# Kernel tuning notes

Measured on AMD Instinct MI355X. Metric: run time of the kernel, lower is better.

Reference implementation:

```python
import jax, jax.numpy as jnp
import numpy as np

GRID_SIZE = 5   # efficient-kan default
K = 3           # spline_order
BATCH = 32768
OBS_DIM = 128
ACTION_DIM = 18
# (in_features, out_features) for the 7 KANLinear layers:
# base: 128->256->256->64 ; adv head: 64->64->18 ; value head: 64->64->1
DIMS = [(OBS_DIM, 256), (256, 256), (256, 64), (64, 64), (64, ACTION_DIM), (64, 64), (64, 1)]


def make_grid(in_f):
    # uniform grid on [-1,1] extended by K knots each side: shape (in_f, GRID_SIZE+2K+1)
    h = 2.0 / GRID_SIZE
    g = jnp.arange(-K, GRID_SIZE + K + 1, dtype=jnp.float32) * h - 1.0
    return jnp.broadcast_to(g, (in_f, g.shape[0]))


def b_splines(x, grid):
    # Cox-de Boor recursion; x: (B, in) -> bases (B, in, GRID_SIZE+K)
    xe = x[:, :, None]
    b = ((xe >= grid[:, :-1]) & (xe < grid[:, 1:])).astype(x.dtype)
    for j in range(1, K + 1):
        left = (xe - grid[:, : -(j + 1)]) / (grid[:, j:-1] - grid[:, : -(j + 1)])
        right = (grid[:, j + 1:] - xe) / (grid[:, j + 1:] - grid[:, 1:-j])
        b = left * b[:, :, :-1] + right * b[:, :, 1:]
    return b


def kan_layer(x, bw, sw, sc):
    # efficient-kan KANLinear: silu base path + spline path with standalone scaler
    grid = make_grid(x.shape[1])
    base = jax.nn.silu(x) @ bw.T                              # (B, out)
    bases = b_splines(x, grid)                                # (B, in, G+K)
    spline = jnp.einsum('big,oig->bo', bases, sw * sc[:, :, None])
    return base + spline


def setup_inputs() -> dict:
    key = jax.random.key(0)
    ks = jax.random.split(key, 1 + 3 * len(DIMS))
    inp = {"x": jax.random.normal(ks[0], (BATCH, OBS_DIM), dtype=jnp.float32)}
    for i, (fin, fout) in enumerate(DIMS):
        inp[f"bw{i}"] = jax.random.normal(ks[1 + 3 * i], (fout, fin), dtype=jnp.float32) / np.sqrt(fin).astype(np.float32)
        inp[f"sw{i}"] = jax.random.normal(ks[2 + 3 * i], (fout, fin, GRID_SIZE + K), dtype=jnp.float32) * (0.1 / np.sqrt(fin).astype(np.float32))
        inp[f"sc{i}"] = 1.0 + 0.1 * jax.random.normal(ks[3 + 3 * i], (fout, fin), dtype=jnp.float32)
    return inp


def reference(x, bw0, sw0, sc0, bw1, sw1, sc1, bw2, sw2, sc2,
              bw3, sw3, sc3, bw4, sw4, sc4, bw5, sw5, sc5, bw6, sw6, sc6):
    h = x
    for bw, sw, sc in [(bw0, sw0, sc0), (bw1, sw1, sc1), (bw2, sw2, sc2)]:
        h = kan_layer(h, bw, sw, sc)
    advantage = kan_layer(kan_layer(h, bw3, sw3, sc3), bw4, sw4, sc4)
    state_value = kan_layer(kan_layer(h, bw5, sw5, sc5), bw6, sw6, sc6)
    return (advantage, state_value)
```

## Files before the change

kernel.cpp:

```cpp
#include <hip/hip_runtime.h>

typedef unsigned short u16;
typedef unsigned int   u32;
typedef unsigned long long u64;
typedef __bf16 bf16;
typedef float f32x4  __attribute__((ext_vector_type(4)));
typedef bf16  bf16x8 __attribute__((ext_vector_type(8)));

__device__ __forceinline__ float bf2f(u16 u){ return (float)__builtin_bit_cast(bf16,u); }
__device__ __forceinline__ u16   f2bf(float f){ return __builtin_bit_cast(u16,(bf16)f); }
__device__ __forceinline__ u32   pkbf(float a,float b){ return (u32)f2bf(a)|((u32)f2bf(b)<<16); }

#define NROWS 32768

__device__ __forceinline__ uint4 basis_pk(float x)
{
  float tp  = __fmaf_rn(x, 2.5f, 5.5f);
  float tpc = fminf(fmaxf(tp, -1.0f), 12.0f);
  float fi  = floorf(tpc);
  float uu  = tpc - fi;
  int   i0  = (int)fi;
  float u2 = uu*uu, u3 = u2*uu, w1 = 1.0f-uu, w2 = w1*w1, w3 = w2*w1;
  float d1 = __fmaf_rn(3.0f, u3, __fmaf_rn(-6.0f, u2, 4.0f));
  float d2 = __fmaf_rn(3.0f, w3, __fmaf_rn(-6.0f, w2, 4.0f));
  u64 dpk = (u64)pkbf(w3, d1) | ((u64)pkbf(d2, u3) << 32);
  int ss = i0*16 - 48;
  u64 A  = dpk << (ss & 63);
  u64 Bv = dpk >> ((64-ss) & 63);
  u64 Cv = dpk << ((ss-64) & 63);
  u64 Dv = dpk >> ((-ss) & 63);
  u64 lo = (ss>=0 && ss<64)   ? A  : ((ss<0 && ss>-64) ? Dv : 0ull);
  u64 hi = (ss>=64 && ss<128) ? Cv : ((ss>0 && ss<64)  ? Bv : 0ull);
  uint4 r; r.x=(u32)lo; r.y=(u32)(lo>>32); r.z=(u32)hi; r.w=(u32)(hi>>32);
  return r;
}

__device__ __forceinline__ void expand9(float x, u16& sil, uint4& bpk)
{
  float s = x * (1.0f/(1.0f+__expf(-x)));
  sil = f2bf(s);
  bpk = basis_pk(x);
}
__device__ __forceinline__ void expand10(float x, u32& spk, uint4& bpk)
{
  float s = x * (1.0f/(1.0f+__expf(-x)));
  u16 uh = f2bf(s);
  u16 ul = f2bf(s - bf2f(uh));
  spk = (u32)uh | ((u32)ul<<16);
  bpk = basis_pk(x);
}

struct PrepArgs {
  const float* bw[7]; const float* sw[7]; const float* sc[7];
  u16* w[7];
  int cin[7]; int coutr[7]; int ntsh[7]; int fmt[7];
  u32 elems[7];
};

__global__ __launch_bounds__(256) void prep_kernel(PrepArgs pa)
{
  u32 idx = blockIdx.x*256 + threadIdx.x;
  int L = 0;
  u32 off = idx;
  while (L < 6 && off >= pa.elems[L]) { off -= pa.elems[L]; ++L; }
  int j    = off & 7;
  int lane = (off>>3) & 63;
  u32 tl   = off >> 9;
  int ntsh = pa.ntsh[L];
  u32 kstep = tl >> ntsh;
  int ntile = (int)(tl & ((1u<<ntsh)-1u));
  int o    = ntile*16 + (lane&15);
  int kpos = (lane>>4)*8 + j;
  int i = 0, g = 0; bool sil;
  if (pa.fmt[L] == 0){
    u32 c = kstep/9u; int r = (int)(kstep - c*9u);
    if (r == 0){ i = (int)c*32 + kpos; sil = true; }
    else { int kl=(r-1)*32+kpos; i=(int)c*32+(kl>>3); g=kl&7; sil = false; }
  } else {
    u32 c = kstep/5u; int r = (int)(kstep - c*5u);
    if (r == 0){ i = (int)c*16 + (kpos>>1); sil = true; }
    else { int kl=(r-1)*32+kpos; i=(int)c*16+(kl>>3); g=kl&7; sil = false; }
  }
  float v = 0.f;
  if (o < pa.coutr[L]) {
    size_t e = (size_t)o*pa.cin[L] + i;
    v = sil ? pa.bw[L][e] : pa.sw[L][e*8+g]*pa.sc[L][e]*0.16666666666666666f;
  }
  pa.w[L][off] = f2bf(v);
}

template<int CIN,int COUT,int GR,int GC,int IN_MODE,int OUT_MODE>
__global__ __launch_bounds__(512,4) void kan_layer(const void* __restrict__ hin_,
    const u16* __restrict__ W, void* __restrict__ hout_)
{
  constexpr int ROWS = 64;
  constexpr int NCH = CIN/32;
  constexpr int TOTK = NCH*9;
  constexpr int NTILES = COUT/16;
  constexpr int MT  = ROWS/(GR*16);
  constexpr int NTL = NTILES/GC;
  static_assert(GR*GC == 8, "wave grid must use all 8 waves");
  static_assert(MT*GR*16 == ROWS, "row coverage");
  static_assert(NTL*GC == NTILES, "col coverage");
  constexpr int SROW=20, BROW=132, BOFF=ROWS*SROW;
  constexpr int CHUNK = BOFF + ROWS*BROW;
  constexpr int WSTEP = NTILES*512;
  __shared__ __align__(16) u32 buf[2][CHUNK];

  const int b0 = blockIdx.x*ROWS;
  const int tid = threadIdx.x;
  const int wave = tid>>6, lane = tid&63, m = lane&15, quad = lane>>4;
  const int rg = wave / GC, cg = wave % GC;
  const int rbase = rg*(MT*16);

  const u16*   __restrict__ hb = (const u16*)hin_;
  const float* __restrict__ hf = (const float*)hin_;

  f32x4 acc[MT][NTL];
#pragma unroll
  for (int a=0;a<MT;++a)
#pragma unroll
    for (int n=0;n<NTL;++n) acc[a][n]=(f32x4){0.f,0.f,0.f,0.f};

  const u16* wq = W + ((size_t)(cg*NTL)*64 + lane)*8;
  bf16x8 bbuf[3][NTL];
  auto loadB = [&](int kstep, bf16x8* dst){
    if (kstep < TOTK){
#pragma unroll
      for (int nt=0; nt<NTL; ++nt)
        dst[nt] = *(const bf16x8*)(wq + nt*512);
    }
    wq += WSTEP;
  };
  loadB(0, bbuf[0]); loadB(1, bbuf[1]);

  float xb[2][4];
  auto loadX = [&](int kc, float* dst){
#pragma unroll
    for (int t=0;t<4;++t){
      int task = t*512+tid, row = task>>5, f = task&31;
      int gi = (b0+row)*CIN + kc*32 + f;
      dst[t] = (IN_MODE==0)? hf[gi] : bf2f(hb[gi]);
    }
  };
  auto expandChunk = [&](const float* xc, u32* dstb){
#pragma unroll
    for (int t=0;t<4;++t){
      int task=t*512+tid, row=task>>5, f=task&31;
      u16 sil; uint4 bpk;
      expand9(xc[t], sil, bpk);
      ((u16*)dstb)[row*(SROW*2) + f] = sil;
      *(uint4*)&dstb[BOFF + row*BROW + f*4] = bpk;
    }
  };

  loadX(0, xb[0]);
  expandChunk(xb[0], buf[0]);
  if (NCH > 1) loadX(1, xb[1]);
  __syncthreads();

  for (int kc=0; kc<NCH; ++kc){
    u32* cur = buf[kc&1];
    u32* nxt = buf[(kc+1)&1];
    if (kc+1 < NCH) expandChunk(xb[(kc+1)&1], nxt);
    if (kc+2 < NCH) loadX(kc+2, xb[kc&1]);
#pragma unroll
    for (int ks=0; ks<9; ++ks){
      const int kstep = kc*9 + ks;
      loadB(kstep+2, bbuf[(ks+2)%3]);
      bf16x8 af[MT];
#pragma unroll
      for (int mt=0; mt<MT; ++mt){
        int row = rbase + mt*16 + m;
        af[mt] = (ks==0)
          ? *(const bf16x8*)&cur[row*SROW + quad*4]
          : *(const bf16x8*)&cur[BOFF + row*BROW + (ks-1)*16 + quad*4];
      }
#pragma unroll
      for (int nt=0; nt<NTL; ++nt)
#pragma unroll
        for (int mt=0; mt<MT; ++mt)
          acc[mt][nt] = __builtin_amdgcn_mfma_f32_16x16x32_bf16(af[mt], bbuf[ks%3][nt], acc[mt][nt],0,0,0);
    }
    __syncthreads();
  }

#pragma unroll
  for (int mt=0; mt<MT; ++mt)
#pragma unroll
    for (int nt=0; nt<NTL; ++nt)
#pragma unroll
      for (int r=0; r<4; ++r){
        size_t off = (size_t)(b0 + rbase + mt*16 + quad*4 + r)*COUT + (cg*NTL+nt)*16 + m;
        if constexpr (OUT_MODE==0) ((float*)hout_)[off] = acc[mt][nt][r];
        else                       ((u16*)hout_)[off]   = f2bf(acc[mt][nt][r]);
      }
}

template<int IN_MODE>
__global__ __launch_bounds__(512,4) void tail2_kernel(const void* __restrict__ h1_,
  const u16* __restrict__ W2, const u16* __restrict__ W3, const u16* __restrict__ W4,
  const u16* __restrict__ W5, const u16* __restrict__ W6,
  float* __restrict__ out_adv, float* __restrict__ out_val)
{
  __shared__ __align__(16) u32 smem[19456];
  float* hH = (float*)smem;
  float* hA = (float*)(smem + 4160);
  float* hV = (float*)(smem + 8320);
  u32*  Aex = smem + 12480;

  const int b0 = blockIdx.x*64;
  const int tid = threadIdx.x;
  const int wave = tid>>6, lane = tid&63, m = lane&15, quad = lane>>4;
  const int rg = wave>>2, cg = wave&3;

  const u16*   __restrict__ hb = (const u16*)h1_;
  const float* __restrict__ hf = (const float*)h1_;

  {
    constexpr int CIN=256, NCH=8, TOTK=72, NTILES=4;
    constexpr int SROW=20, BROW=132, BOFF=64*SROW, CHUNK=BOFF+64*BROW;
    f32x4 acc[2];
    acc[0]=(f32x4){0,0,0,0}; acc[1]=(f32x4){0,0,0,0};
    const u16* wq = W2 + ((size_t)cg*64 + lane)*8;
    bf16x8 bb[3];
    auto loadB = [&](int kstep, bf16x8* dst){
      if (kstep < TOTK) *dst = *(const bf16x8*)wq;
      wq += NTILES*512;
    };
    loadB(0,&bb[0]); loadB(1,&bb[1]);
    float xb[2][4];
    auto loadX = [&](int kc, float* dst){
#pragma unroll
      for (int t=0;t<4;++t){
        int task=t*512+tid, row=task>>5, f=task&31;
        int gi=(b0+row)*CIN + kc*32 + f;
        dst[t] = (IN_MODE==0)? hf[gi] : bf2f(hb[gi]);
      }
    };
    auto expandChunk = [&](const float* xc, u32* dstb){
#pragma unroll
      for (int t=0;t<4;++t){
        int task=t*512+tid, row=task>>5, f=task&31;
        u16 sil; uint4 bpk;
        expand9(xc[t], sil, bpk);
        ((u16*)dstb)[row*(SROW*2)+f] = sil;
        *(uint4*)&dstb[BOFF + row*BROW + f*4] = bpk;
      }
    };
    loadX(0, xb[0]);
    expandChunk(xb[0], smem);
    loadX(1, xb[1]);
    __syncthreads();
    for (int kc=0; kc<NCH; ++kc){
      u32* cur = smem + (kc&1)*CHUNK;
      u32* nxt = smem + ((kc+1)&1)*CHUNK;
      if (kc+1 < NCH) expandChunk(xb[(kc+1)&1], nxt);
      if (kc+2 < NCH) loadX(kc+2, xb[kc&1]);
#pragma unroll
      for (int ks=0; ks<9; ++ks){
        loadB(kc*9+ks+2, &bb[(ks+2)%3]);
        bf16x8 af[2];
#pragma unroll
        for (int mt=0; mt<2; ++mt){
          int row = rg*32 + mt*16 + m;
          af[mt] = (ks==0)
            ? *(const bf16x8*)&cur[row*SROW + quad*4]
            : *(const bf16x8*)&cur[BOFF + row*BROW + (ks-1)*16 + quad*4];
        }
#pragma unroll
        for (int mt=0; mt<2; ++mt)
          acc[mt] = __builtin_amdgcn_mfma_f32_16x16x32_bf16(af[mt], bb[ks%3], acc[mt],0,0,0);
      }
      __syncthreads();
    }
#pragma unroll
    for (int mt=0; mt<2; ++mt)
#pragma unroll
      for (int r=0;r<4;++r)
        hH[(rg*32 + mt*16 + quad*4 + r)*65 + cg*16 + m] = acc[mt][r];
  }
  __syncthreads();

  constexpr int SROW=20, BROW=68, BOFF=64*20;

  f32x4 a3[2], a5[2];
#pragma unroll
  for (int mt=0;mt<2;++mt){ a3[mt]=(f32x4){0,0,0,0}; a5[mt]=(f32x4){0,0,0,0}; }

  const u16* w3q = W3 + ((size_t)cg*64 + lane)*8;
  const u16* w5q = W5 + ((size_t)cg*64 + lane)*8;
  bf16x8 w3b[3], w5b[3];
  auto loadB2 = [&](int kstep, int d){
    if (kstep < 20){
      w3b[d] = *(const bf16x8*)w3q;
      w5b[d] = *(const bf16x8*)w5q;
    }
    w3q += 4*512; w5q += 4*512;
  };
  loadB2(0,0); loadB2(1,1);

  for (int kc=0; kc<4; ++kc){
#pragma unroll
    for (int t=0;t<2;++t){
      int task=t*512+tid, row=task>>4, f=task&15;
      u32 spk; uint4 bpk;
      expand10(hH[row*65 + kc*16 + f], spk, bpk);
      Aex[row*SROW + f] = spk;
      *(uint4*)&Aex[BOFF + row*BROW + f*4] = bpk;
    }
    __syncthreads();
#pragma unroll
    for (int ks=0; ks<5; ++ks){
      loadB2(kc*5+ks+2, 2);
      bf16x8 af[2];
#pragma unroll
      for (int mt=0; mt<2; ++mt){
        int row = rg*32 + mt*16 + m;
        af[mt] = (ks==0)
          ? *(const bf16x8*)&Aex[row*SROW + quad*4]
          : *(const bf16x8*)&Aex[BOFF + row*BROW + (ks-1)*16 + quad*4];
      }
#pragma unroll
      for (int mt=0; mt<2; ++mt){
        a3[mt] = __builtin_amdgcn_mfma_f32_16x16x32_bf16(af[mt], w3b[0], a3[mt],0,0,0);
        a5[mt] = __builtin_amdgcn_mfma_f32_16x16x32_bf16(af[mt], w5b[0], a5[mt],0,0,0);
      }
      w3b[0]=w3b[1]; w3b[1]=w3b[2]; w5b[0]=w5b[1]; w5b[1]=w5b[2];
    }
    __syncthreads();
  }
#pragma unroll
  for (int mt=0;mt<2;++mt)
#pragma unroll
    for (int r=0;r<4;++r){
      int row = rg*32 + mt*16 + quad*4 + r;
      hA[row*65 + cg*16 + m] = a3[mt][r];
      hV[row*65 + cg*16 + m] = a5[mt][r];
    }
  __syncthreads();

  f32x4 a4[2];
#pragma unroll
  for (int mt=0;mt<2;++mt) a4[mt]=(f32x4){0,0,0,0};
  const u16* w4q = W4 + ((size_t)cg*64 + lane)*8;
  bf16x8 w4b[3];
  auto loadB4 = [&](int kstep, int d){
    if (kstep < 20) w4b[d] = *(const bf16x8*)w4q;
    w4q += 4*512;
  };
  loadB4(0,0); loadB4(1,1);
  for (int kc=0; kc<4; ++kc){
#pragma unroll
    for (int t=0;t<2;++t){
      int task=t*512+tid, row=task>>4, f=task&15;
      u32 spk; uint4 bpk;
      expand10(hA[row*65 + kc*16 + f], spk, bpk);
      Aex[row*SROW + f] = spk;
      *(uint4*)&Aex[BOFF + row*BROW + f*4] = bpk;
    }
    __syncthreads();
#pragma unroll
    for (int ks=0; ks<5; ++ks){
      loadB4(kc*5+ks+2, 2);
      bf16x8 af[2];
#pragma unroll
      for (int mt=0; mt<2; ++mt){
        int row = rg*32 + mt*16 + m;
        af[mt] = (ks==0)
          ? *(const bf16x8*)&Aex[row*SROW + quad*4]
          : *(const bf16x8*)&Aex[BOFF + row*BROW + (ks-1)*16 + quad*4];
      }
#pragma unroll
      for (int mt=0; mt<2; ++mt)
        a4[mt] = __builtin_amdgcn_mfma_f32_16x16x32_bf16(af[mt], w4b[0], a4[mt],0,0,0);
      w4b[0]=w4b[1]; w4b[1]=w4b[2];
    }
    __syncthreads();
  }
  {
    int col = cg*16 + m;
    if (col < 18){
#pragma unroll
      for (int mt=0;mt<2;++mt)
#pragma unroll
        for (int r=0;r<4;++r)
          out_adv[(size_t)(b0 + rg*32 + mt*16 + quad*4 + r)*18 + col] = a4[mt][r];
    }
  }

  f32x4 a6[2];
#pragma unroll
  for (int mt=0;mt<2;++mt) a6[mt]=(f32x4){0,0,0,0};
  const u16* w6q = W6 + ((size_t)cg*64 + lane)*8;
  bf16x8 w6b[3];
  auto loadB6 = [&](int kstep, int d){
    if (kstep < 20) w6b[d] = *(const bf16x8*)w6q;
    w6q += 4*512;
  };
  loadB6(0,0); loadB6(1,1);
  for (int kc=0; kc<4; ++kc){
#pragma unroll
    for (int t=0;t<2;++t){
      int task=t*512+tid, row=task>>4, f=task&15;
      u32 spk; uint4 bpk;
      expand10(hV[row*65 + kc*16 + f], spk, bpk);
      Aex[row*SROW + f] = spk;
      *(uint4*)&Aex[BOFF + row*BROW + f*4] = bpk;
    }
    __syncthreads();
#pragma unroll
    for (int ks=0; ks<5; ++ks){
      loadB6(kc*5+ks+2, 2);
      bf16x8 af[2];
#pragma unroll
      for (int mt=0; mt<2; ++mt){
        int row = rg*32 + mt*16 + m;
        af[mt] = (ks==0)
          ? *(const bf16x8*)&Aex[row*SROW + quad*4]
          : *(const bf16x8*)&Aex[BOFF + row*BROW + (ks-1)*16 + quad*4];
      }
#pragma unroll
      for (int mt=0; mt<2; ++mt)
        a6[mt] = __builtin_amdgcn_mfma_f32_16x16x32_bf16(af[mt], w6b[0], a6[mt],0,0,0);
      w6b[0]=w6b[1]; w6b[1]=w6b[2];
    }
    __syncthreads();
  }
  if (cg==0 && m==0){
#pragma unroll
    for (int mt=0;mt<2;++mt)
#pragma unroll
      for (int r=0;r<4;++r)
        out_val[b0 + rg*32 + mt*16 + quad*4 + r] = a6[mt][r];
  }
}

extern "C" void kernel_launch(void* const* d_in, const int* in_sizes, int n_in,
                              void* d_out, int out_size, void* d_ws, size_t ws_size,
                              hipStream_t stream)
{
  (void)in_sizes; (void)n_in; (void)out_size;
  char* ws = (char*)d_ws;

  const size_t wbytes[7] = {589824u, 1179648u, 294912u, 81920u, 81920u, 81920u, 81920u};
  const bool midf32 = ws_size >= 77889536u;

  u16* W[7];
  char *h0, *h1;
  if (midf32) {
    h0 = ws;
    h1 = h0 + 33554432u;
    size_t off = 75497472u;
    for (int l=0;l<7;++l){ W[l] = (u16*)(ws+off); off += wbytes[l]; }
  } else {
    h0 = ws;
    h1 = h0 + 16777216u;
    size_t off = 37748736u;
    for (int l=0;l<7;++l){ W[l] = (u16*)(ws+off); off += wbytes[l]; }
  }

  PrepArgs pa;
  const int cins[7]   = {128,256,256,64,64,64,64};
  const int coutr[7]  = {256,256,64,64,18,64,1};
  const int ntsh[7]   = {4,4,2,2,2,2,2};
  const int fmts[7]   = {0,0,0,1,1,1,1};
  const u32 elems[7]  = {294912u,589824u,147456u,40960u,40960u,40960u,40960u};
  for (int l=0;l<7;++l){
    pa.bw[l] = (const float*)d_in[1+3*l];
    pa.sw[l] = (const float*)d_in[2+3*l];
    pa.sc[l] = (const float*)d_in[3+3*l];
    pa.w[l]  = W[l];
    pa.cin[l]=cins[l]; pa.coutr[l]=coutr[l]; pa.ntsh[l]=ntsh[l]; pa.fmt[l]=fmts[l];
    pa.elems[l]=elems[l];
  }
  prep_kernel<<<4672, 256, 0, stream>>>(pa);

  dim3 g64(NROWS/64), bl(512);
  float* out_adv = (float*)d_out;
  float* out_val = (float*)d_out + (size_t)NROWS*18;
  if (midf32) {
    kan_layer<128,256,1,8,0,0><<<g64,bl,0,stream>>>(d_in[0], W[0], h0);
    kan_layer<256,256,1,8,0,0><<<g64,bl,0,stream>>>(h0, W[1], h1);
    tail2_kernel<0><<<g64,bl,0,stream>>>(h1, W[2], W[3], W[4], W[5], W[6], out_adv, out_val);
  } else {
    kan_layer<128,256,1,8,0,1><<<g64,bl,0,stream>>>(d_in[0], W[0], h0);
    kan_layer<256,256,1,8,1,1><<<g64,bl,0,stream>>>(h0, W[1], h1);
    tail2_kernel<1><<<g64,bl,0,stream>>>(h1, W[2], W[3], W[4], W[5], W[6], out_adv, out_val);
  }
}
```

Before: 221.7 us.

## Fuse three layer kernels into one persistent-per-tile mega kernel

Merges the two wide KAN layer kernels and the tail kernel into a single launch where each block processes its 64-row tile through all layers in sequence, sharing one shared-memory buffer. This removes two kernel launches and the inter-kernel gaps, and lets each block reread its own intermediate rows while they may still be cached in L2. Intermediates still round-trip through global memory. Register pressure becomes the maximum across all phases, which may lower occupancy, and the __restrict__ qualifiers on the intermediate pointers are dropped.

```diff
diff --git a/kernel.cpp b/kernel.cpp
--- a/kernel.cpp
+++ b/kernel.cpp
@@ -89,36 +89,27 @@
   pa.w[L][off] = f2bf(v);
 }
 
-template<int CIN,int COUT,int GR,int GC,int IN_MODE,int OUT_MODE>
-__global__ __launch_bounds__(512,4) void kan_layer(const void* __restrict__ hin_,
-    const u16* __restrict__ W, void* __restrict__ hout_)
-{
-  constexpr int ROWS = 64;
+template<int CIN,int COUT,int IN_MODE,int OUT_MODE>
+__device__ __forceinline__ void kan_phase(u32* smem, int b0, int tid,
+    const void* hin_, const u16* __restrict__ W, void* hout_)
+{
   constexpr int NCH = CIN/32;
   constexpr int TOTK = NCH*9;
   constexpr int NTILES = COUT/16;
-  constexpr int MT  = ROWS/(GR*16);
-  constexpr int NTL = NTILES/GC;
-  static_assert(GR*GC == 8, "wave grid must use all 8 waves");
-  static_assert(MT*GR*16 == ROWS, "row coverage");
-  static_assert(NTL*GC == NTILES, "col coverage");
-  constexpr int SROW=20, BROW=132, BOFF=ROWS*SROW;
-  constexpr int CHUNK = BOFF + ROWS*BROW;
+  constexpr int NTL = NTILES/8;
+  constexpr int SROW=20, BROW=132, BOFF=64*SROW;
+  constexpr int CHUNK = BOFF + 64*BROW;
   constexpr int WSTEP = NTILES*512;
-  __shared__ __align__(16) u32 buf[2][CHUNK];
-
-  const int b0 = blockIdx.x*ROWS;
-  const int tid = threadIdx.x;
+
   const int wave = tid>>6, lane = tid&63, m = lane&15, quad = lane>>4;
-  const int rg = wave / GC, cg = wave % GC;
-  const int rbase = rg*(MT*16);
-
-  const u16*   __restrict__ hb = (const u16*)hin_;
-  const float* __restrict__ hf = (const float*)hin_;
-
-  f32x4 acc[MT][NTL];
-#pragma unroll
-  for (int a=0;a<MT;++a)
+  const int cg = wave;
+
+  const u16*   hb = (const u16*)hin_;
+  const float* hf = (const float*)hin_;
+
+  f32x4 acc[4][NTL];
+#pragma unroll
+  for (int a=0;a<4;++a)
 #pragma unroll
     for (int n=0;n<NTL;++n) acc[a][n]=(f32x4){0.f,0.f,0.f,0.f};
 
@@ -155,23 +146,22 @@
   };
 
   loadX(0, xb[0]);
-  expandChunk(xb[0], buf[0]);
+  expandChunk(xb[0], smem);
   if (NCH > 1) loadX(1, xb[1]);
   __syncthreads();
 
   for (int kc=0; kc<NCH; ++kc){
-    u32* cur = buf[kc&1];
-    u32* nxt = buf[(kc+1)&1];
+    u32* cur = smem + (kc&1)*CHUNK;
+    u32* nxt = smem + ((kc+1)&1)*CHUNK;
     if (kc+1 < NCH) expandChunk(xb[(kc+1)&1], nxt);
     if (kc+2 < NCH) loadX(kc+2, xb[kc&1]);
 #pragma unroll
     for (int ks=0; ks<9; ++ks){
-      const int kstep = kc*9 + ks;
-      loadB(kstep+2, bbuf[(ks+2)%3]);
-      bf16x8 af[MT];
-#pragma unroll
-      for (int mt=0; mt<MT; ++mt){
-        int row = rbase + mt*16 + m;
+      loadB(kc*9+ks+2, bbuf[(ks+2)%3]);
+      bf16x8 af[4];
+#pragma unroll
+      for (int mt=0; mt<4; ++mt){
+        int row = mt*16 + m;
         af[mt] = (ks==0)
           ? *(const bf16x8*)&cur[row*SROW + quad*4]
           : *(const bf16x8*)&cur[BOFF + row*BROW + (ks-1)*16 + quad*4];
@@ -179,43 +169,41 @@
 #pragma unroll
       for (int nt=0; nt<NTL; ++nt)
 #pragma unroll
-        for (int mt=0; mt<MT; ++mt)
+        for (int mt=0; mt<4; ++mt)
           acc[mt][nt] = __builtin_amdgcn_mfma_f32_16x16x32_bf16(af[mt], bbuf[ks%3][nt], acc[mt][nt],0,0,0);
     }
     __syncthreads();
   }
 
 #pragma unroll
-  for (int mt=0; mt<MT; ++mt)
+  for (int mt=0; mt<4; ++mt)
 #pragma unroll
     for (int nt=0; nt<NTL; ++nt)
 #pragma unroll
       for (int r=0; r<4; ++r){
-        size_t off = (size_t)(b0 + rbase + mt*16 + quad*4 + r)*COUT + (cg*NTL+nt)*16 + m;
+        size_t off = (size_t)(b0 + mt*16 + quad*4 + r)*COUT + (cg*NTL+nt)*16 + m;
         if constexpr (OUT_MODE==0) ((float*)hout_)[off] = acc[mt][nt][r];
         else                       ((u16*)hout_)[off]   = f2bf(acc[mt][nt][r]);
       }
 }
 
 template<int IN_MODE>
-__global__ __launch_bounds__(512,4) void tail2_kernel(const void* __restrict__ h1_,
+__device__ __forceinline__ void tail_body(u32* smem, int b0, int tid,
+  const void* h1_,
   const u16* __restrict__ W2, const u16* __restrict__ W3, const u16* __restrict__ W4,
   const u16* __restrict__ W5, const u16* __restrict__ W6,
   float* __restrict__ out_adv, float* __restrict__ out_val)
 {
-  __shared__ __align__(16) u32 smem[19456];
   float* hH = (float*)smem;
   float* hA = (float*)(smem + 4160);
   float* hV = (float*)(smem + 8320);
   u32*  Aex = smem + 12480;
 
-  const int b0 = blockIdx.x*64;
-  const int tid = threadIdx.x;
   const int wave = tid>>6, lane = tid&63, m = lane&15, quad = lane>>4;
   const int rg = wave>>2, cg = wave&3;
 
-  const u16*   __restrict__ hb = (const u16*)h1_;
-  const float* __restrict__ hf = (const float*)h1_;
+  const u16*   hb = (const u16*)h1_;
+  const float* hf = (const float*)h1_;
 
   {
     constexpr int CIN=256, NCH=8, TOTK=72, NTILES=4;
@@ -436,6 +424,25 @@
   }
 }
 
+template<int MID>
+__global__ __launch_bounds__(512,4) void mega_kernel(
+  const float* __restrict__ x, void* h0_, void* h1_,
+  const u16* __restrict__ W0, const u16* __restrict__ W1, const u16* __restrict__ W2,
+  const u16* __restrict__ W3, const u16* __restrict__ W4,
+  const u16* __restrict__ W5, const u16* __restrict__ W6,
+  float* __restrict__ out_adv, float* __restrict__ out_val)
+{
+  __shared__ __align__(16) u32 smem[19456];
+  const int b0 = blockIdx.x*64;
+  const int tid = threadIdx.x;
+
+  kan_phase<128,256,0,MID>(smem, b0, tid, x, W0, h0_);
+  __syncthreads();
+  kan_phase<256,256,MID,MID>(smem, b0, tid, h0_, W1, h1_);
+  __syncthreads();
+  tail_body<MID>(smem, b0, tid, h1_, W2, W3, W4, W5, W6, out_adv, out_val);
+}
+
 extern "C" void kernel_launch(void* const* d_in, const int* in_sizes, int n_in,
                               void* d_out, int out_size, void* d_ws, size_t ws_size,
                               hipStream_t stream)
@@ -480,12 +487,10 @@
   float* out_adv = (float*)d_out;
   float* out_val = (float*)d_out + (size_t)NROWS*18;
   if (midf32) {
-    kan_layer<128,256,1,8,0,0><<<g64,bl,0,stream>>>(d_in[0], W[0], h0);
-    kan_layer<256,256,1,8,0,0><<<g64,bl,0,stream>>>(h0, W[1], h1);
-    tail2_kernel<0><<<g64,bl,0,stream>>>(h1, W[2], W[3], W[4], W[5], W[6], out_adv, out_val);
+    mega_kernel<0><<<g64,bl,0,stream>>>((const float*)d_in[0], h0, h1,
+      W[0],W[1],W[2],W[3],W[4],W[5],W[6], out_adv, out_val);
   } else {
-    kan_layer<128,256,1,8,0,1><<<g64,bl,0,stream>>>(d_in[0], W[0], h0);
-    kan_layer<256,256,1,8,1,1><<<g64,bl,0,stream>>>(h0, W[1], h1);
-    tail2_kernel<1><<<g64,bl,0,stream>>>(h1, W[2], W[3], W[4], W[5], W[6], out_adv, out_val);
-  }
-}
+    mega_kernel<1><<<g64,bl,0,stream>>>((const float*)d_in[0], h0, h1,
+      W[0],W[1],W[2],W[3],W[4],W[5],W[6], out_adv, out_val);
+  }
+}
```

After: 226.5 us. 1.02x slower.
